# Performance work log

Hardware: AMD Instinct MI355X
Metric: run time of the kernel (lower is better)

## Reference

```python
import jax, jax.numpy as jnp
import numpy as np

EPS = 1e-5
NEG_SLOPE = 0.2

def _conv(x, w, b, stride, pad):
    y = jax.lax.conv_general_dilated(x, w, (stride, stride), ((pad, pad), (pad, pad)),
                                     dimension_numbers=('NCHW', 'OIHW', 'NCHW'))
    return y + b[None, :, None, None]

def _conv_transpose(x, w, b):
    # PyTorch ConvTranspose2d(k=3, s=2, p=1, output_padding=1): equivalent to a
    # lhs-dilated conv with padding (k-1-p, k-1-p+op) = (1, 2). w is stored in the
    # already-flipped OIHW layout (out_ch, in_ch, 3, 3).
    y = jax.lax.conv_general_dilated(x, w, (1, 1), ((1, 2), (1, 2)), lhs_dilation=(2, 2),
                                     dimension_numbers=('NCHW', 'OIHW', 'NCHW'))
    return y + b[None, :, None, None]

def _inorm(x):
    # InstanceNorm2d, affine=False, biased variance over (H, W)
    m = jnp.mean(x, axis=(2, 3), keepdims=True)
    v = jnp.mean((x - m) ** 2, axis=(2, 3), keepdims=True)
    return (x - m) * jax.lax.rsqrt(v + EPS)

def _lrelu(x):
    return jnp.where(x >= 0, x, NEG_SLOPE * x)

def _reflect_pad1(x):
    return jnp.pad(x, ((0, 0), (0, 0), (1, 1), (1, 1)), mode='reflect')


def setup_inputs() -> dict:
    key = jax.random.key(0)
    ks = jax.random.split(key, 12)
    B, H, W, S = 8, 256, 256, 19
    inp = jax.random.normal(ks[0], (B, 3, H, W), dtype=jnp.float32)
    # one-hot semantic map (float, 0/1) like the repo's segmaps
    labels = jax.random.randint(ks[1], (B, H, W), 0, S)
    segmap = jax.nn.one_hot(labels, S, axis=1, dtype=jnp.float32)

    def w(k, o, i):
        return jax.random.normal(k, (o, i, 3, 3), dtype=jnp.float32) * (1.0 / np.sqrt(i * 9))

    return {
        'input': inp, 'segmap': segmap,
        'w0': w(ks[2], 32, 3),    'b0': jnp.zeros((32,), jnp.float32),
        'w1': w(ks[3], 64, 32),   'b1': jnp.zeros((64,), jnp.float32),
        'w2': w(ks[4], 128, 64),  'b2': jnp.zeros((128,), jnp.float32),
        'wt': w(ks[5], 256, 128), 'bt': jnp.zeros((256,), jnp.float32),
        'w3': w(ks[6], 512, 256), 'b3': jnp.zeros((512,), jnp.float32),
    }


def reference(input, segmap, w0, b0, w1, b1, w2, b2, wt, bt, w3, b3):
    # CNN backbone
    x = _conv(_reflect_pad1(input), w0, b0, 1, 0)   # [B,32,256,256]
    x = _lrelu(_inorm(x))
    x = _conv(x, w1, b1, 2, 1)                       # [B,64,128,128]
    x = _lrelu(_inorm(x))
    x = _conv(x, w2, b2, 2, 1)                       # [B,128,64,64]
    x = _lrelu(_inorm(x))
    x = _conv_transpose(x, wt, bt)                   # [B,256,128,128]
    x = _lrelu(_inorm(x))
    codes = jnp.tanh(_conv(_reflect_pad1(x), w3, b3, 1, 0))  # [B,512,128,128]

    # nearest-neighbor downsample of segmap to codes' spatial size (PyTorch floor rule)
    B, C, Hc, Wc = codes.shape
    Hs, Ws = segmap.shape[2], segmap.shape[3]
    hi = (jnp.arange(Hc) * Hs) // Hc
    wi = (jnp.arange(Wc) * Ws) // Wc
    seg = segmap[:, :, hi[:, None], wi[None, :]]     # [B,S,Hc,Wc]

    # fused segment mean pooling (replaces nested masked_select loop)
    m = (seg != 0).astype(codes.dtype)
    sums = jnp.einsum('bchw,bshw->bsc', codes, m)    # [B,S,C]
    cnt = jnp.sum(m, axis=(2, 3))[..., None]          # [B,S,1]
    return jnp.where(cnt > 0, sums / jnp.maximum(cnt, 1.0), 0.0)
```

## Files before the change

### kernel.cpp

```cpp
#include <hip/hip_runtime.h>


#define B 8

typedef __attribute__((ext_vector_type(8))) short short8;
typedef __attribute__((ext_vector_type(4))) float f32x4;

static __device__ __forceinline__ unsigned short f2bf(float f) {
  union { float f; unsigned u; } v;
  v.f = f;
  unsigned r = v.u + 0x7fffu + ((v.u >> 16) & 1u);
  return (unsigned short)(r >> 16);
}
static __device__ __forceinline__ float bf2f(unsigned short h) {
  union { unsigned u; float f; } v;
  v.u = (unsigned)h << 16;
  return v.f;
}
static __device__ __forceinline__ float tanh_fast(float x) {
  float ax = fabsf(x);
  ax = fminf(ax, 20.f);
  const float e = __expf(-2.f * ax);
  const float t = (1.f - e) / (1.f + e);
  return __builtin_copysignf(t, x);
}

static __device__ __forceinline__ void gload_lds16(const unsigned short* g,
                                                   unsigned short* l) {
  __builtin_amdgcn_global_load_lds(
      (const __attribute__((address_space(1))) unsigned int*)(const void*)g,
      (__attribute__((address_space(3))) unsigned int*)(void*)l, 16, 0, 0);
}

__global__ __launch_bounds__(256) void conv0_kernel(
    const float* __restrict__ in, const float* __restrict__ w,
    const float* __restrict__ bias, float* __restrict__ out) {
  __shared__ float sw[32 * 27 + 32];
  for (int i = threadIdx.x; i < 32 * 27; i += 256) sw[i] = w[i];
  if (threadIdx.x < 32) sw[32 * 27 + threadIdx.x] = bias[threadIdx.x];
  __syncthreads();
  const int b = blockIdx.y;
  const int p = blockIdx.x * 256 + threadIdx.x;
  const int y = p >> 8, x = p & 255;
  const float* inb = in + (size_t)b * 3 * 65536;
  float v[27];
#pragma unroll
  for (int c = 0; c < 3; ++c) {
#pragma unroll
    for (int ky = 0; ky < 3; ++ky) {
      int iy = y + ky - 1;
      iy = iy < 0 ? -iy : (iy > 255 ? 510 - iy : iy);
#pragma unroll
      for (int kx = 0; kx < 3; ++kx) {
        int ix = x + kx - 1;
        ix = ix < 0 ? -ix : (ix > 255 ? 510 - ix : ix);
        v[c * 9 + ky * 3 + kx] = inb[c * 65536 + iy * 256 + ix];
      }
    }
  }
  float* ob = out + (size_t)b * 32 * 65536 + p;
#pragma unroll
  for (int co = 0; co < 32; ++co) {
    float a = sw[32 * 27 + co];
#pragma unroll
    for (int k = 0; k < 27; ++k) a = fmaf(v[k], sw[co * 27 + k], a);
    ob[(size_t)co * 65536] = a;
  }
}

__global__ __launch_bounds__(256) void inorm_lrelu_kernel(float* __restrict__ x,
                                                          int HW) {
  const size_t base = (size_t)blockIdx.x * HW;
  float4* p = (float4*)(x + base);
  const int n4 = HW >> 2;
  float s = 0.f, q = 0.f;
  for (int i = threadIdx.x; i < n4; i += 256) {
    float4 v = p[i];
    s += (v.x + v.y) + (v.z + v.w);
    q += (v.x * v.x + v.y * v.y) + (v.z * v.z + v.w * v.w);
  }
  __shared__ float rs[256], rq[256];
  rs[threadIdx.x] = s;
  rq[threadIdx.x] = q;
  __syncthreads();
  for (int st = 128; st > 0; st >>= 1) {
    if (threadIdx.x < st) {
      rs[threadIdx.x] += rs[threadIdx.x + st];
      rq[threadIdx.x] += rq[threadIdx.x + st];
    }
    __syncthreads();
  }
  const float m = rs[0] / (float)HW;
  float var = rq[0] / (float)HW - m * m;
  var = var < 0.f ? 0.f : var;
  const float r = rsqrtf(var + 1e-5f);
  for (int i = threadIdx.x; i < n4; i += 256) {
    float4 v = p[i];
    v.x = (v.x - m) * r; v.x = v.x >= 0.f ? v.x : 0.2f * v.x;
    v.y = (v.y - m) * r; v.y = v.y >= 0.f ? v.y : 0.2f * v.y;
    v.z = (v.z - m) * r; v.z = v.z >= 0.f ? v.z : 0.2f * v.z;
    v.w = (v.w - m) * r; v.w = v.w >= 0.f ? v.w : 0.2f * v.w;
    p[i] = v;
  }
}

__global__ __launch_bounds__(256) void transpose_x0_kernel(
    const float* __restrict__ x0, unsigned short* __restrict__ Xp0) {
  const int b = blockIdx.y;
  const int p0 = blockIdx.x * 64;
  __shared__ unsigned short T[32][66];
  const float* src = x0 + (size_t)b * 32 * 65536;
  const int t = threadIdx.x;
#pragma unroll
  for (int r = 0; r < 8; ++r) {
    const int ci_l = r * 4 + (t >> 6);
    const int p_l = t & 63;
    T[ci_l][p_l] = f2bf(src[(size_t)ci_l * 65536 + p0 + p_l]);
  }
  __syncthreads();
  unsigned short* dst = Xp0 + (size_t)b * 258 * 258 * 32;
  const int p_l = t >> 2;
  const int c0 = (t & 3) * 8;
  union { short8 v; unsigned short u[8]; } pk;
#pragma unroll
  for (int j = 0; j < 8; ++j) pk.u[j] = T[c0 + j][p_l];
  const int p = p0 + p_l;
  const int yy = p >> 8, xx = p & 255;
  *(short8*)(dst + ((size_t)(yy + 1) * 258 + (xx + 1)) * 32 + c0) = pk.v;
}

__global__ __launch_bounds__(256) void zpad0_kernel(unsigned short* __restrict__ Xp0) {
  const int b = blockIdx.x;
  unsigned short* Xb = Xp0 + (size_t)b * 258 * 258 * 32;
  const short8 z = {0, 0, 0, 0, 0, 0, 0, 0};
  for (int i = threadIdx.x; i < 258 * 4; i += 256) {
    const int c = i >> 2, q = (i & 3) * 8;
    *(short8*)(Xb + ((size_t)0 * 258 + c) * 32 + q) = z;
    *(short8*)(Xb + ((size_t)c * 258 + 0) * 32 + q) = z;
  }
}

__global__ __launch_bounds__(256) void w1prep_kernel(const float* __restrict__ w1,
                                                     unsigned short* __restrict__ w1b) {
  const int i = blockIdx.x * 256 + threadIdx.x;
  if (i >= 9 * 64 * 32) return;
  const int e = i & 7, lane = (i >> 3) & 63, cot = (i >> 9) & 3, tap = i >> 11;
  const int co = cot * 16 + (lane & 15);
  const int ci = (lane >> 4) * 8 + e;
  w1b[i] = f2bf(w1[((size_t)co * 32 + ci) * 9 + tap]);
}

__global__ __launch_bounds__(256, 3) void conv1_mfma_kernel(
    const unsigned short* __restrict__ Xp0, const unsigned short* __restrict__ w1b,
    const float* __restrict__ b1, float* __restrict__ x1) {
  const int raw = blockIdx.x;
  const int swz = (raw & 7) * 128 + (raw >> 3);
  const int b = swz >> 7;
  const int oy = swz & 127;

  __shared__ unsigned short Asw1[3084 * 8];

  const int t = threadIdx.x;
  const int lane = t & 63;
  const int wave = t >> 6;
  const int wm = wave >> 1, wn = wave & 1;
  const int lg = lane >> 4, lr = lane & 15;
  const int wslot = wave * 64;

  const unsigned short* Xb = Xp0 + (size_t)b * 258 * 258 * 32;

#pragma unroll
  for (int k = 0; k < 13; ++k) {
    int s;
    bool act = true;
    if (k < 12) s = t + k * 256;
    else { s = 3072 + lane; act = (wave == 0 && lane < 12); }
    const int r = s / 1028, rm = s % 1028, c = rm >> 2, hs = rm & 3;
    const int h = hs ^ ((c >> 1) & 3);
    const unsigned short* gsrc = Xb + ((size_t)(2 * oy + r) * 258 + c) * 32 + h * 8;
    unsigned short* ldst = (k < 12) ? (Asw1 + (size_t)(k * 256 + wslot) * 8)
                                    : (Asw1 + (size_t)3072 * 8);
    if (act) gload_lds16(gsrc, ldst);
  }

  f32x4 acc[4][2];
#pragma unroll
  for (int mt = 0; mt < 4; ++mt)
#pragma unroll
    for (int nt = 0; nt < 2; ++nt) {
      f32x4 z = {0.f, 0.f, 0.f, 0.f};
      acc[mt][nt] = z;
    }
  __syncthreads();

  const unsigned short* w1l = w1b + (size_t)lane * 8;
#pragma unroll
  for (int tap = 0; tap < 9; ++tap) {
    const int ky = tap / 3, kx = tap % 3;
    short8 bf[2];
#pragma unroll
    for (int nt = 0; nt < 2; ++nt)
      bf[nt] = *(const short8*)(w1l + (size_t)(tap * 4 + wn * 2 + nt) * 512);
    short8 af[4];
#pragma unroll
    for (int mt = 0; mt < 4; ++mt) {
      const int c = 2 * (wm * 64 + mt * 16 + lr) + kx;
      const int hh = lg ^ ((c >> 1) & 3);
      af[mt] = *(const short8*)(Asw1 + (size_t)(ky * 1028 + c * 4 + hh) * 8);
    }
#pragma unroll
    for (int nt = 0; nt < 2; ++nt)
#pragma unroll
      for (int mt = 0; mt < 4; ++mt)
        acc[mt][nt] = __builtin_amdgcn_mfma_f32_16x16x32_bf16(
            af[mt], bf[nt], acc[mt][nt], 0, 0, 0);
  }

  float b1v[2];
#pragma unroll
  for (int nt = 0; nt < 2; ++nt) b1v[nt] = b1[wn * 32 + nt * 16 + lr];
#pragma unroll
  for (int mt = 0; mt < 4; ++mt) {
#pragma unroll
    for (int nt = 0; nt < 2; ++nt) {
      const int px = wm * 64 + mt * 16 + lg * 4;
      const int co = wn * 32 + nt * 16 + lr;
      float4 v;
      v.x = acc[mt][nt][0] + b1v[nt];
      v.y = acc[mt][nt][1] + b1v[nt];
      v.z = acc[mt][nt][2] + b1v[nt];
      v.w = acc[mt][nt][3] + b1v[nt];
      *(float4*)(x1 + ((size_t)(b * 64 + co)) * 16384 + oy * 128 + px) = v;
    }
  }
}

__global__ __launch_bounds__(256) void transpose_x1_kernel(
    const float* __restrict__ x1, unsigned short* __restrict__ Xp1) {
  const int b = blockIdx.y;
  const int p0 = blockIdx.x * 64;
  __shared__ unsigned short T[64][66];
  const float* src = x1 + (size_t)b * 64 * 16384;
  const int t = threadIdx.x;
#pragma unroll
  for (int r = 0; r < 16; ++r) {
    const int ci_l = r * 4 + (t >> 6);
    const int p_l = t & 63;
    T[ci_l][p_l] = f2bf(src[(size_t)ci_l * 16384 + p0 + p_l]);
  }
  __syncthreads();
  unsigned short* dst = Xp1 + (size_t)b * 130 * 130 * 64;
#pragma unroll
  for (int r = 0; r < 2; ++r) {
    const int p_l = r * 32 + (t >> 3);
    const int c0 = (t & 7) * 8;
    union { short8 v; unsigned short u[8]; } pk;
#pragma unroll
    for (int j = 0; j < 8; ++j) pk.u[j] = T[c0 + j][p_l];
    const int p = p0 + p_l;
    const int yy = p >> 7, xx = p & 127;
    *(short8*)(dst + ((size_t)(yy + 1) * 130 + (xx + 1)) * 64 + c0) = pk.v;
  }
}

__global__ __launch_bounds__(256) void zpad1_kernel(unsigned short* __restrict__ Xp1) {
  const int b = blockIdx.x;
  unsigned short* Xb = Xp1 + (size_t)b * 130 * 130 * 64;
  const short8 z = {0, 0, 0, 0, 0, 0, 0, 0};
  for (int i = threadIdx.x; i < 130 * 8; i += 256) {
    const int c = i >> 3, q = (i & 7) * 8;
    *(short8*)(Xb + ((size_t)0 * 130 + c) * 64 + q) = z;
    *(short8*)(Xb + ((size_t)c * 130 + 0) * 64 + q) = z;
  }
}

__global__ __launch_bounds__(256) void w2prep_kernel(const float* __restrict__ w2,
                                                     unsigned short* __restrict__ w2b) {
  const int i = blockIdx.x * 256 + threadIdx.x;
  if (i >= 9 * 128 * 64) return;
  const int e = i & 7, lane = (i >> 3) & 63, cc = (i >> 9) & 1;
  const int cot = (i >> 10) & 7, tap = i >> 13;
  const int co = cot * 16 + (lane & 15);
  const int ci = cc * 32 + (lane >> 4) * 8 + e;
  w2b[i] = f2bf(w2[((size_t)co * 64 + ci) * 9 + tap]);
}

__global__ __launch_bounds__(256, 3) void conv2_mfma_kernel(
    const unsigned short* __restrict__ Xp1, const unsigned short* __restrict__ w2b,
    const float* __restrict__ b2, float* __restrict__ x2) {
  const int raw = blockIdx.x;
  const int swz = (raw & 7) * 64 + (raw >> 3);
  const int b = swz >> 6;
  const int oy = swz & 63;

  __shared__ unsigned short Asw2[3096 * 8];

  const int t = threadIdx.x;
  const int lane = t & 63;
  const int wave = t >> 6;
  const int wm = wave >> 1, wn = wave & 1;
  const int lg = lane >> 4, lr = lane & 15;
  const int wslot = wave * 64;

  const unsigned short* Xb = Xp1 + (size_t)b * 130 * 130 * 64;

#pragma unroll
  for (int k = 0; k < 13; ++k) {
    int s;
    bool act = true;
    if (k < 12) s = t + k * 256;
    else { s = 3072 + lane; act = (wave == 0 && lane < 24); }
    const int r = s / 1032, rm = s % 1032, c = rm >> 3, hs = rm & 7;
    const int h = hs ^ ((c >> 1) & 7);
    const unsigned short* gsrc = Xb + ((size_t)(2 * oy + r) * 130 + c) * 64 + h * 8;
    unsigned short* ldst = (k < 12) ? (Asw2 + (size_t)(k * 256 + wslot) * 8)
                                    : (Asw2 + (size_t)3072 * 8);
    if (act) gload_lds16(gsrc, ldst);
  }

  f32x4 acc[2][4];
#pragma unroll
  for (int mt = 0; mt < 2; ++mt)
#pragma unroll
    for (int nt = 0; nt < 4; ++nt) {
      f32x4 z = {0.f, 0.f, 0.f, 0.f};
      acc[mt][nt] = z;
    }
  __syncthreads();

  const unsigned short* w2l = w2b + (size_t)lane * 8;
#pragma unroll
  for (int tap = 0; tap < 9; ++tap) {
    const int ky = tap / 3, kx = tap % 3;
#pragma unroll
    for (int cc = 0; cc < 2; ++cc) {
      short8 bf[4];
#pragma unroll
      for (int nt = 0; nt < 4; ++nt)
        bf[nt] = *(const short8*)(
            w2l + (size_t)((tap * 8 + wn * 4 + nt) * 2 + cc) * 512);
      short8 af[2];
#pragma unroll
      for (int mt = 0; mt < 2; ++mt) {
        const int c = 2 * (wm * 32 + mt * 16 + lr) + kx;
        const int hh = (cc * 4 + lg) ^ ((c >> 1) & 7);
        af[mt] = *(const short8*)(Asw2 + (size_t)(ky * 1032 + c * 8 + hh) * 8);
      }
#pragma unroll
      for (int nt = 0; nt < 4; ++nt)
#pragma unroll
        for (int mt = 0; mt < 2; ++mt)
          acc[mt][nt] = __builtin_amdgcn_mfma_f32_16x16x32_bf16(
              af[mt], bf[nt], acc[mt][nt], 0, 0, 0);
    }
  }

  float b2v[4];
#pragma unroll
  for (int nt = 0; nt < 4; ++nt) b2v[nt] = b2[wn * 64 + nt * 16 + lr];
#pragma unroll
  for (int mt = 0; mt < 2; ++mt) {
#pragma unroll
    for (int nt = 0; nt < 4; ++nt) {
      const int px = wm * 32 + mt * 16 + lg * 4;
      const int co = wn * 64 + nt * 16 + lr;
      float4 v;
      v.x = acc[mt][nt][0] + b2v[nt];
      v.y = acc[mt][nt][1] + b2v[nt];
      v.z = acc[mt][nt][2] + b2v[nt];
      v.w = acc[mt][nt][3] + b2v[nt];
      *(float4*)(x2 + ((size_t)(b * 128 + co)) * 4096 + oy * 64 + px) = v;
    }
  }
}

__global__ __launch_bounds__(256) void transpose_x2_kernel(
    const float* __restrict__ x2, unsigned short* __restrict__ X2p) {
  const int b = blockIdx.y;
  const int p0 = (blockIdx.x & 63) * 64;
  const int ci0 = (blockIdx.x >> 6) * 64;
  __shared__ unsigned short T[64][66];
  const float* src = x2 + (size_t)b * 128 * 4096;
  const int t = threadIdx.x;
#pragma unroll
  for (int r = 0; r < 16; ++r) {
    const int ci_l = r * 4 + (t >> 6);
    const int p_l = t & 63;
    T[ci_l][p_l] = f2bf(src[(size_t)(ci0 + ci_l) * 4096 + p0 + p_l]);
  }
  __syncthreads();
  unsigned short* dst = X2p + (size_t)b * 65 * 65 * 128;
#pragma unroll
  for (int r = 0; r < 2; ++r) {
    const int p_l = r * 32 + (t >> 3);
    const int c0 = (t & 7) * 8;
    union { short8 v; unsigned short u[8]; } pk;
#pragma unroll
    for (int j = 0; j < 8; ++j) pk.u[j] = T[c0 + j][p_l];
    const int p = p0 + p_l;
    const int yy = p >> 6, xx = p & 63;
    *(short8*)(dst + ((size_t)yy * 65 + xx) * 128 + ci0 + c0) = pk.v;
  }
}

__global__ __launch_bounds__(256) void zpad_x2_kernel(unsigned short* __restrict__ X2p) {
  const int b = blockIdx.x;
  unsigned short* Xb = X2p + (size_t)b * 65 * 65 * 128;
  for (int i = threadIdx.x; i < 129 * 128; i += 256) {
    const int j = i >> 7, ci = i & 127;
    size_t off;
    if (j < 65) off = ((size_t)64 * 65 + j) * 128 + ci;
    else off = ((size_t)(j - 65) * 65 + 64) * 128 + ci;
    Xb[off] = 0;
  }
}

__global__ __launch_bounds__(256) void wtprep_kernel(const float* __restrict__ wt,
                                                     unsigned short* __restrict__ Wtb2) {
  const int i = blockIdx.x * 256 + threadIdx.x;
  if (i >= 9 * 256 * 128) return;
  const int e = i & 7, lane = (i >> 3) & 63, c4 = (i >> 9) & 3;
  const int cot = (i >> 11) & 15, tap = i >> 15;
  const int co = cot * 16 + (lane & 15);
  const int ci = c4 * 32 + (lane >> 4) * 8 + e;
  Wtb2[i] = f2bf(wt[((size_t)co * 128 + ci) * 9 + tap]);
}

__global__ __launch_bounds__(256, 3) void convt_mfma_kernel(
    const unsigned short* __restrict__ X2p, const unsigned short* __restrict__ Wtb2,
    const float* __restrict__ bt, unsigned short* __restrict__ Y) {
  const int raw = blockIdx.x;
  const int swz = (raw & 7) * 256 + (raw >> 3);
  const int b = swz >> 8;
  const int rem = swz & 255;
  const int cls = rem >> 6;
  const int sy = rem & 63;
  const int py = cls & 1, px = cls >> 1;

  const int kyA = py ? 0 : 1, kxA = px ? 0 : 1;
  int tk[4], tdy[4], tdx[4];
  int ntaps = 0;
  tk[ntaps] = kyA * 3 + kxA; tdy[ntaps] = 0; tdx[ntaps] = 0; ++ntaps;
  if (px) { tk[ntaps] = kyA * 3 + 2; tdy[ntaps] = 0; tdx[ntaps] = 1; ++ntaps; }
  if (py) { tk[ntaps] = 6 + kxA; tdy[ntaps] = 1; tdx[ntaps] = 0; ++ntaps; }
  if (py && px) { tk[ntaps] = 8; tdy[ntaps] = 1; tdx[ntaps] = 1; ++ntaps; }

  constexpr int CS = 36;
  constexpr int BUFN = 2 * 65 * CS;
  __shared__ unsigned short As2[2 * BUFN];

  const int t = threadIdx.x;
  const int lane = t & 63;
  const int wn = t >> 6;
  const int lg = lane >> 4, lr = lane & 15;
  const int co_w = wn * 64;

  const unsigned short* Xb = X2p + (size_t)b * 65 * 65 * 128;

  int dof0, dof1, dof2;
  const unsigned short *sp0, *sp1, *sp2;
  bool sv2;
  {
    const int i0 = t, i1 = t + 256, i2 = t + 512;
    const int r0 = i0 / 260, c0_ = (i0 % 260) >> 2, h0 = i0 & 3;
    const int r1 = i1 / 260, c1_ = (i1 % 260) >> 2, h1 = i1 & 3;
    sv2 = i2 < 520;
    const int i2c = sv2 ? i2 : 512;
    const int r2 = i2c / 260, c2_ = (i2c % 260) >> 2, h2 = i2c & 3;
    dof0 = (r0 * 65 + c0_) * CS + h0 * 8;
    dof1 = (r1 * 65 + c1_) * CS + h1 * 8;
    dof2 = (r2 * 65 + c2_) * CS + h2 * 8;
    sp0 = Xb + ((size_t)(sy + r0) * 65 + c0_) * 128 + h0 * 8;
    sp1 = Xb + ((size_t)(sy + r1) * 65 + c1_) * 128 + h1 * 8;
    sp2 = Xb + ((size_t)(sy + r2) * 65 + c2_) * 128 + h2 * 8;
  }

  f32x4 acc[4][4];
#pragma unroll
  for (int mt = 0; mt < 4; ++mt)
#pragma unroll
    for (int nt = 0; nt < 4; ++nt) {
      f32x4 z = {0.f, 0.f, 0.f, 0.f};
      acc[mt][nt] = z;
    }

  {
    const short8 a = *(const short8*)sp0;
    const short8 bq = *(const short8*)sp1;
    short8 cq;
    if (sv2) cq = *(const short8*)sp2;
    *(short8*)(As2 + dof0) = a;
    *(short8*)(As2 + dof1) = bq;
    if (sv2) *(short8*)(As2 + dof2) = cq;
  }
  __syncthreads();

  const unsigned short* wlane = Wtb2 + (size_t)lane * 8;

  for (int c8 = 0; c8 < 4; ++c8) {
    short8 n0, n1, n2;
    if (c8 < 3) {
      const int cn = (c8 + 1) * 32;
      n0 = *(const short8*)(sp0 + cn);
      n1 = *(const short8*)(sp1 + cn);
      if (sv2) n2 = *(const short8*)(sp2 + cn);
    }
    const unsigned short* Ab = As2 + (c8 & 1) * BUFN;
    for (int tp = 0; tp < ntaps; ++tp) {
      const int dy = tdy[tp], dx = tdx[tp];
      short8 af[4];
#pragma unroll
      for (int mt = 0; mt < 4; ++mt)
        af[mt] = *(const short8*)(Ab + (dy * 65 + mt * 16 + lr + dx) * CS + lg * 8);
      const unsigned short* wt_ =
          wlane + (size_t)(((tk[tp] * 16 + wn * 4) * 4) + c8) * 512;
#pragma unroll
      for (int nt = 0; nt < 4; ++nt) {
        const short8 bf = *(const short8*)(wt_ + (size_t)nt * (4 * 512));
#pragma unroll
        for (int mt = 0; mt < 4; ++mt)
          acc[mt][nt] = __builtin_amdgcn_mfma_f32_16x16x32_bf16(
              af[mt], bf, acc[mt][nt], 0, 0, 0);
      }
    }
    if (c8 < 3) {
      unsigned short* Db = As2 + ((c8 + 1) & 1) * BUFN;
      *(short8*)(Db + dof0) = n0;
      *(short8*)(Db + dof1) = n1;
      if (sv2) *(short8*)(Db + dof2) = n2;
    }
    __syncthreads();
  }

  const int oy = 2 * sy + py;
  unsigned short* Yb = Y + ((size_t)b * 16384 + (size_t)oy * 128 + px) * 256;
  float bco[4];
#pragma unroll
  for (int nt = 0; nt < 4; ++nt) bco[nt] = bt[co_w + nt * 16 + lr];
#pragma unroll
  for (int mt = 0; mt < 4; ++mt) {
#pragma unroll
    for (int r = 0; r < 4; ++r) {
      const int sx = mt * 16 + lg * 4 + r;
      unsigned short* yp = Yb + (size_t)(2 * sx) * 256 + co_w + lr;
#pragma unroll
      for (int nt = 0; nt < 4; ++nt)
        yp[nt * 16] = f2bf(acc[mt][nt][r] + bco[nt]);
    }
  }
}

__global__ __launch_bounds__(256) void inorm_stats_kernel(
    const unsigned short* __restrict__ Y, float* __restrict__ ssum,
    float* __restrict__ ssq) {
  const int b = blockIdx.y, sl = blockIdx.x;
  const int t = threadIdx.x;
  const int rg = t >> 5;
  const int c0 = (t & 31) * 8;
  const unsigned short* base = Y + ((size_t)b * 16384 + sl * 256) * 256;
  float s[8], q[8];
#pragma unroll
  for (int j = 0; j < 8; ++j) { s[j] = 0.f; q[j] = 0.f; }
  for (int i = 0; i < 32; ++i) {
    union { short8 v; unsigned short u[8]; } pk;
    pk.v = *(const short8*)(base + (size_t)(rg + i * 8) * 256 + c0);
#pragma unroll
    for (int j = 0; j < 8; ++j) {
      const float v = bf2f(pk.u[j]);
      s[j] += v;
      q[j] += v * v;
    }
  }
  __shared__ float sm[2][8][256];
#pragma unroll
  for (int j = 0; j < 8; ++j) {
    sm[0][rg][c0 + j] = s[j];
    sm[1][rg][c0 + j] = q[j];
  }
  __syncthreads();
  float ts = 0.f, tq = 0.f;
#pragma unroll
  for (int g = 0; g < 8; ++g) {
    ts += sm[0][g][t];
    tq += sm[1][g][t];
  }
  atomicAdd(&ssum[b * 256 + t], ts);
  atomicAdd(&ssq[b * 256 + t], tq);
}

__global__ __launch_bounds__(256) void inorm_apply_kernel(
    const unsigned short* __restrict__ Y, const float* __restrict__ ssum,
    const float* __restrict__ ssq, unsigned short* __restrict__ Xpad) {
  const int b = blockIdx.y, sl = blockIdx.x;
  const int t = threadIdx.x;
  const int rg = t >> 5;
  const int c0 = (t & 31) * 8;
  float m[8], r[8];
#pragma unroll
  for (int j = 0; j < 8; ++j) {
    const float mm = ssum[b * 256 + c0 + j] * (1.f / 16384.f);
    float var = ssq[b * 256 + c0 + j] * (1.f / 16384.f) - mm * mm;
    var = var < 0.f ? 0.f : var;
    m[j] = mm;
    r[j] = rsqrtf(var + 1e-5f);
  }
  const unsigned short* base = Y + ((size_t)b * 16384 + sl * 256) * 256;
  unsigned short* dstb = Xpad + (size_t)b * 130 * 130 * 256;
  for (int i = 0; i < 32; ++i) {
    const int row = sl * 256 + rg + i * 8;
    const int yy = row >> 7, xx = row & 127;
    union { short8 v; unsigned short u[8]; } pk;
    pk.v = *(const short8*)(base + (size_t)(rg + i * 8) * 256 + c0);
#pragma unroll
    for (int j = 0; j < 8; ++j) {
      float v = bf2f(pk.u[j]);
      v = (v - m[j]) * r[j];
      v = v >= 0.f ? v : 0.2f * v;
      pk.u[j] = f2bf(v);
    }
    *(short8*)(dstb + ((size_t)(yy + 1) * 130 + (xx + 1)) * 256 + c0) = pk.v;
  }
}

__global__ __launch_bounds__(256) void pad_rows_kernel(unsigned short* __restrict__ Xp) {
  const int b = blockIdx.x >> 1, side = blockIdx.x & 1;
  unsigned short* Xb = Xp + (size_t)b * 130 * 130 * 256;
  const int dr = side ? 129 : 0, sr = side ? 127 : 2;
  for (int i = threadIdx.x; i < 4096; i += 256) {
    const int c = 1 + (i >> 5), o = (i & 31) * 8;
    *(short8*)(Xb + ((size_t)dr * 130 + c) * 256 + o) =
        *(const short8*)(Xb + ((size_t)sr * 130 + c) * 256 + o);
  }
}
__global__ __launch_bounds__(256) void pad_cols_kernel(unsigned short* __restrict__ Xp) {
  const int b = blockIdx.x >> 1, side = blockIdx.x & 1;
  unsigned short* Xb = Xp + (size_t)b * 130 * 130 * 256;
  const int dc = side ? 129 : 0, sc = side ? 127 : 2;
  for (int i = threadIdx.x; i < 130 * 32; i += 256) {
    const int r = i >> 5, o = (i & 31) * 8;
    *(short8*)(Xb + ((size_t)r * 130 + dc) * 256 + o) =
        *(const short8*)(Xb + ((size_t)r * 130 + sc) * 256 + o);
  }
}

__global__ __launch_bounds__(256) void wprep_kernel(const float* __restrict__ w3,
                                                    unsigned short* __restrict__ Wb2) {
  const int i = blockIdx.x * 256 + threadIdx.x;
  if (i >= 9 * 512 * 256) return;
  const int e = i & 7, lane = (i >> 3) & 63, c8 = (i >> 9) & 7;
  const int cot = (i >> 12) & 31, tap = i >> 17;
  const int co = cot * 16 + (lane & 15);
  const int ci = c8 * 32 + (lane >> 4) * 8 + e;
  Wb2[i] = f2bf(w3[((size_t)co * 256 + ci) * 9 + tap]);
}

__global__ __launch_bounds__(256) void label_kernel(
    const float* __restrict__ segmap, int* __restrict__ labels,
    float* __restrict__ cnt) {
  const int b = blockIdx.y;
  const int p = blockIdx.x * 256 + threadIdx.x;
  const int i = p >> 7, j = p & 127;
  const float* sp = segmap + (size_t)b * 19 * 65536 + (2 * i) * 256 + 2 * j;
  int lab = 0;
#pragma unroll
  for (int s = 0; s < 19; ++s)
    if (sp[(size_t)s * 65536] != 0.f) lab = s;
  labels[b * 16384 + p] = lab;
  atomicAdd(&cnt[b * 19 + lab], 1.0f);
}

__global__ __launch_bounds__(256, 3) void conv3_mfma_pool_kernel(
    const unsigned short* __restrict__ Xpad, const unsigned short* __restrict__ Wb2,
    const float* __restrict__ bias, const int* __restrict__ labels,
    float* __restrict__ sums) {
  const int raw = blockIdx.x;
  const int swz = (raw & 7) * 512 + (raw >> 3);
  const int b = swz >> 9;
  const int rem = swz & 511;
  const int y = rem >> 2;
  const int coq = rem & 3;

  constexpr int SLOTS = 1600;
  __shared__ unsigned short Asw[2 * SLOTS * 8];
  float* lsum = (float*)Asw;

  const int t = threadIdx.x;
  const int lane = t & 63;
  const int wave = t >> 6;
  const int wm = wave >> 1;
  const int wn = wave & 1;
  const int lg = lane >> 4, lr = lane & 15;
  const int co_w = coq * 128 + wn * 64;

  const unsigned short* Xb = Xpad + (size_t)b * 130 * 130 * 256;

  const unsigned short* sp[7];
  {
#pragma unroll
    for (int k = 0; k < 7; ++k) {
      int s;
      if (k < 6) s = t + k * 256;
      else s = (t < 24) ? (1536 + t) : 1536;
      const int r = s / 520, rm = s % 520, c = rm >> 2, hs = rm & 3;
      const int E = r * 130 + c;
      const int h = hs ^ ((E >> 1) & 3);
      sp[k] = Xb + ((size_t)(y + r) * 130 + c) * 256 + h * 8;
    }
  }

  f32x4 acc[4][4];
#pragma unroll
  for (int mt = 0; mt < 4; ++mt)
#pragma unroll
    for (int nt = 0; nt < 4; ++nt) {
      f32x4 z = {0.f, 0.f, 0.f, 0.f};
      acc[mt][nt] = z;
    }

  const unsigned short* wlane = Wb2 + (size_t)lane * 8;

  const int wslot = wave * 64;
#define STAGE(bufSel, off)                                                   \
  {                                                                          \
    unsigned short* base_ = Asw + (bufSel) * (SLOTS * 8);                    \
    gload_lds16(sp[0] + (off), base_ + (size_t)wslot * 8);                   \
    gload_lds16(sp[1] + (off), base_ + (size_t)(wslot + 256) * 8);           \
    gload_lds16(sp[2] + (off), base_ + (size_t)(wslot + 512) * 8);           \
    gload_lds16(sp[3] + (off), base_ + (size_t)(wslot + 768) * 8);           \
    gload_lds16(sp[4] + (off), base_ + (size_t)(wslot + 1024) * 8);          \
    gload_lds16(sp[5] + (off), base_ + (size_t)(wslot + 1280) * 8);          \
    if (wave == 0 && lane < 24)                                              \
      gload_lds16(sp[6] + (off), base_ + (size_t)1536 * 8);                  \
  }

  STAGE(0, 0)
  __syncthreads();

  for (int c8 = 0; c8 < 8; ++c8) {
    if (c8 < 7) STAGE((c8 + 1) & 1, (c8 + 1) * 32)
    const unsigned short* Ab = Asw + (c8 & 1) * (SLOTS * 8);
#pragma unroll
    for (int ky = 0; ky < 3; ++ky) {
#pragma unroll
      for (int kx = 0; kx < 3; ++kx) {
        const unsigned short* wt_ =
            wlane +
            (size_t)(((ky * 3 + kx) * 32 + coq * 8 + wn * 4) * 8 + c8) * 512;
        short8 bfv[4];
#pragma unroll
        for (int nt = 0; nt < 4; ++nt)
          bfv[nt] = *(const short8*)(wt_ + (size_t)nt * (8 * 512));
        short8 af[4];
#pragma unroll
        for (int mt = 0; mt < 4; ++mt) {
          const int E = ky * 130 + wm * 64 + mt * 16 + lr + kx;
          const int hh = lg ^ ((E >> 1) & 3);
          af[mt] = *(const short8*)(Ab + (size_t)E * 32 + hh * 8);
        }
#pragma unroll
        for (int nt = 0; nt < 4; ++nt) {
#pragma unroll
          for (int mt = 0; mt < 4; ++mt)
            acc[mt][nt] = __builtin_amdgcn_mfma_f32_16x16x32_bf16(
                af[mt], bfv[nt], acc[mt][nt], 0, 0, 0);
        }
      }
    }
    __syncthreads();
  }
#undef STAGE

  for (int i = t; i < 19 * 128; i += 256) lsum[i] = 0.f;
  __syncthreads();

  const int* labp = labels + b * 16384 + y * 128;
  float bco[4];
#pragma unroll
  for (int nt = 0; nt < 4; ++nt) bco[nt] = bias[co_w + nt * 16 + lr];
#pragma unroll
  for (int mt = 0; mt < 4; ++mt) {
#pragma unroll
    for (int r = 0; r < 4; ++r) {
      const int lab = labp[wm * 64 + mt * 16 + lg * 4 + r];
#pragma unroll
      for (int nt = 0; nt < 4; ++nt) {
        const float v = tanh_fast(acc[mt][nt][r] + bco[nt]);
        atomicAdd(&lsum[lab * 128 + wn * 64 + nt * 16 + lr], v);
      }
    }
  }
  __syncthreads();
  for (int i = t; i < 19 * 128; i += 256) {
    const float v = lsum[i];
    if (v != 0.f) {
      const int sI = i >> 7, c = i & 127;
      atomicAdd(&sums[((size_t)b * 19 + sI) * 512 + coq * 128 + c], v);
    }
  }
}

__global__ __launch_bounds__(256) void finalize_kernel(
    const float* __restrict__ sums, const float* __restrict__ cnt,
    float* __restrict__ out) {
  const int i = blockIdx.x * 256 + threadIdx.x;
  if (i >= B * 19 * 512) return;
  const int bs = i >> 9;
  const float c = cnt[bs];
  out[i] = c > 0.f ? sums[i] / fmaxf(c, 1.f) : 0.f;
}

extern "C" void kernel_launch(void* const* d_in, const int* in_sizes, int n_in,
                              void* d_out, int out_size, void* d_ws,
                              size_t ws_size, hipStream_t stream) {
  const float* input = (const float*)d_in[0];
  const float* segmap = (const float*)d_in[1];
  const float* w0 = (const float*)d_in[2];
  const float* b0 = (const float*)d_in[3];
  const float* w1 = (const float*)d_in[4];
  const float* b1 = (const float*)d_in[5];
  const float* w2 = (const float*)d_in[6];
  const float* b2 = (const float*)d_in[7];
  const float* wt = (const float*)d_in[8];
  const float* bt = (const float*)d_in[9];
  const float* w3 = (const float*)d_in[10];
  const float* b3 = (const float*)d_in[11];
  float* out = (float*)d_out;

  float* ws = (float*)d_ws;
  float* x0 = ws;
  float* x1 = x0 + 16777216;
  float* x2 = x1 + 8388608;
  unsigned short* X2p = (unsigned short*)(x2 + 4194304);
  unsigned short* Y = X2p + 4326400;
  float* sums = (float*)(Y + 33554432);
  float* cnt = sums + 77824;
  float* ssum = cnt + 152;
  float* ssq = ssum + 2048;
  int* labels = (int*)(ssq + 2048);
  unsigned short* Wb2 = (unsigned short*)(labels + 131072);
  unsigned short* Wtb2 = Wb2 + 1179648;
  unsigned short* w1b = Wtb2 + 294912;
  unsigned short* w2b = w1b + 18432;
  unsigned short* Xpad = (unsigned short*)ws;
  unsigned short* Xp0 = Y;
  unsigned short* Xp1 = Y + 17040384;

  hipMemsetAsync(sums, 0, (77824 + 152 + 2048 + 2048) * sizeof(float), stream);

  wprep_kernel<<<dim3((9 * 512 * 256 + 255) / 256), 256, 0, stream>>>(w3, Wb2);
  wtprep_kernel<<<dim3((9 * 256 * 128 + 255) / 256), 256, 0, stream>>>(wt, Wtb2);
  w1prep_kernel<<<dim3((9 * 64 * 32 + 255) / 256), 256, 0, stream>>>(w1, w1b);
  w2prep_kernel<<<dim3((9 * 128 * 64 + 255) / 256), 256, 0, stream>>>(w2, w2b);

  conv0_kernel<<<dim3(256, B), 256, 0, stream>>>(input, w0, b0, x0);
  inorm_lrelu_kernel<<<dim3(B * 32), 256, 0, stream>>>(x0, 65536);
  transpose_x0_kernel<<<dim3(1024, B), 256, 0, stream>>>(x0, Xp0);
  zpad0_kernel<<<dim3(B), 256, 0, stream>>>(Xp0);
  conv1_mfma_kernel<<<dim3(1024), 256, 0, stream>>>(Xp0, w1b, b1, x1);
  inorm_lrelu_kernel<<<dim3(B * 64), 256, 0, stream>>>(x1, 16384);
  transpose_x1_kernel<<<dim3(256, B), 256, 0, stream>>>(x1, Xp1);
  zpad1_kernel<<<dim3(B), 256, 0, stream>>>(Xp1);
  conv2_mfma_kernel<<<dim3(512), 256, 0, stream>>>(Xp1, w2b, b2, x2);
  inorm_lrelu_kernel<<<dim3(B * 128), 256, 0, stream>>>(x2, 4096);
  transpose_x2_kernel<<<dim3(128, B), 256, 0, stream>>>(x2, X2p);
  zpad_x2_kernel<<<dim3(B), 256, 0, stream>>>(X2p);
  convt_mfma_kernel<<<dim3(2048), 256, 0, stream>>>(X2p, Wtb2, bt, Y);
  inorm_stats_kernel<<<dim3(64, B), 256, 0, stream>>>(Y, ssum, ssq);
  inorm_apply_kernel<<<dim3(64, B), 256, 0, stream>>>(Y, ssum, ssq, Xpad);
  pad_rows_kernel<<<dim3(2 * B), 256, 0, stream>>>(Xpad);
  pad_cols_kernel<<<dim3(2 * B), 256, 0, stream>>>(Xpad);
  label_kernel<<<dim3(64, B), 256, 0, stream>>>(segmap, labels, cnt);
  conv3_mfma_pool_kernel<<<dim3(4096), 256, 0, stream>>>(Xpad, Wb2, b3, labels, sums);
  finalize_kernel<<<dim3((B * 19 * 512 + 255) / 256), 256, 0, stream>>>(sums, cnt, out);
}
```

Measured before the change: 961.8 us.

## Write bf16 NHWC directly from convs, fuse instance-norm stats into epilogues

conv0, conv1 and conv2 now write bf16 channels-last padded tensors directly. This removes the fp32 NCHW intermediates and the separate transpose kernels. Instance norm for these layers is split into a pixel-major stats kernel with atomics plus an in-place apply kernel. The transposed conv accumulates per-channel sum and sum-of-squares in its epilogue, which drops the separate stats pass, and its input staging now uses direct global-to-LDS loads into a swizzled layout without double buffering. The risks are that stats are now computed from bf16-rounded values, and conv1/conv2 issue scattered 2-byte stores.

```diff
diff --git a/kernel.cpp b/kernel.cpp
--- a/kernel.cpp
+++ b/kernel.cpp
@@ -34,7 +34,7 @@
 
 __global__ __launch_bounds__(256) void conv0_kernel(
     const float* __restrict__ in, const float* __restrict__ w,
-    const float* __restrict__ bias, float* __restrict__ out) {
+    const float* __restrict__ bias, unsigned short* __restrict__ Xp0) {
   __shared__ float sw[32 * 27 + 32];
   for (int i = threadIdx.x; i < 32 * 27; i += 256) sw[i] = w[i];
   if (threadIdx.x < 32) sw[32 * 27 + threadIdx.x] = bias[threadIdx.x];
@@ -58,75 +58,100 @@
       }
     }
   }
-  float* ob = out + (size_t)b * 32 * 65536 + p;
-#pragma unroll
-  for (int co = 0; co < 32; ++co) {
-    float a = sw[32 * 27 + co];
-#pragma unroll
-    for (int k = 0; k < 27; ++k) a = fmaf(v[k], sw[co * 27 + k], a);
-    ob[(size_t)co * 65536] = a;
-  }
-}
-
-__global__ __launch_bounds__(256) void inorm_lrelu_kernel(float* __restrict__ x,
-                                                          int HW) {
-  const size_t base = (size_t)blockIdx.x * HW;
-  float4* p = (float4*)(x + base);
-  const int n4 = HW >> 2;
-  float s = 0.f, q = 0.f;
-  for (int i = threadIdx.x; i < n4; i += 256) {
-    float4 v = p[i];
-    s += (v.x + v.y) + (v.z + v.w);
-    q += (v.x * v.x + v.y * v.y) + (v.z * v.z + v.w * v.w);
-  }
-  __shared__ float rs[256], rq[256];
-  rs[threadIdx.x] = s;
-  rq[threadIdx.x] = q;
+  unsigned short* ob =
+      Xp0 + ((size_t)b * 258 * 258 + (size_t)(y + 1) * 258 + (x + 1)) * 32;
+#pragma unroll
+  for (int q = 0; q < 4; ++q) {
+    union { short8 v8; unsigned short u[8]; } pk;
+#pragma unroll
+    for (int j = 0; j < 8; ++j) {
+      const int co = q * 8 + j;
+      float a = sw[32 * 27 + co];
+#pragma unroll
+      for (int k = 0; k < 27; ++k) a = fmaf(v[k], sw[co * 27 + k], a);
+      pk.u[j] = f2bf(a);
+    }
+    *(short8*)(ob + q * 8) = pk.v8;
+  }
+}
+
+template <int C, int WLOG, int STR, int SH, int ITER>
+__global__ __launch_bounds__(256) void stats_px_kernel(
+    const unsigned short* __restrict__ X, float* __restrict__ ssum,
+    float* __restrict__ ssq) {
+  constexpr int G = C / 8;
+  constexpr int R = 256 / G;
+  const int b = blockIdx.y;
+  const int t = threadIdx.x;
+  const int rg = t / G;
+  const int cg = (t % G) * 8;
+  const int px0 = blockIdx.x * (R * ITER);
+  const unsigned short* Xb = X + (size_t)b * STR * STR * C;
+  float s[8], q[8];
+#pragma unroll
+  for (int j = 0; j < 8; ++j) { s[j] = 0.f; q[j] = 0.f; }
+  for (int i = 0; i < ITER; ++i) {
+    const int p = px0 + i * R + rg;
+    const int yy = p >> WLOG, xx = p & ((1 << WLOG) - 1);
+    union { short8 v8; unsigned short u[8]; } pk;
+    pk.v8 = *(const short8*)(Xb + ((size_t)(yy + SH) * STR + (xx + SH)) * C + cg);
+#pragma unroll
+    for (int j = 0; j < 8; ++j) {
+      const float v = bf2f(pk.u[j]);
+      s[j] += v;
+      q[j] += v * v;
+    }
+  }
+  __shared__ float sm[2][R][C];
+#pragma unroll
+  for (int j = 0; j < 8; ++j) {
+    sm[0][rg][cg + j] = s[j];
+    sm[1][rg][cg + j] = q[j];
+  }
   __syncthreads();
-  for (int st = 128; st > 0; st >>= 1) {
-    if (threadIdx.x < st) {
-      rs[threadIdx.x] += rs[threadIdx.x + st];
-      rq[threadIdx.x] += rq[threadIdx.x + st];
-    }
-    __syncthreads();
-  }
-  const float m = rs[0] / (float)HW;
-  float var = rq[0] / (float)HW - m * m;
-  var = var < 0.f ? 0.f : var;
-  const float r = rsqrtf(var + 1e-5f);
-  for (int i = threadIdx.x; i < n4; i += 256) {
-    float4 v = p[i];
-    v.x = (v.x - m) * r; v.x = v.x >= 0.f ? v.x : 0.2f * v.x;
-    v.y = (v.y - m) * r; v.y = v.y >= 0.f ? v.y : 0.2f * v.y;
-    v.z = (v.z - m) * r; v.z = v.z >= 0.f ? v.z : 0.2f * v.z;
-    v.w = (v.w - m) * r; v.w = v.w >= 0.f ? v.w : 0.2f * v.w;
-    p[i] = v;
-  }
-}
-
-__global__ __launch_bounds__(256) void transpose_x0_kernel(
-    const float* __restrict__ x0, unsigned short* __restrict__ Xp0) {
+  if (t < C) {
+    float ts = 0.f, tq = 0.f;
+    for (int g2 = 0; g2 < R; ++g2) {
+      ts += sm[0][g2][t];
+      tq += sm[1][g2][t];
+    }
+    atomicAdd(&ssum[b * C + t], ts);
+    atomicAdd(&ssq[b * C + t], tq);
+  }
+}
+
+template <int C, int WLOG, int STR, int SH>
+__global__ __launch_bounds__(256) void apply_px_kernel(
+    unsigned short* __restrict__ X, const float* __restrict__ ssum,
+    const float* __restrict__ ssq) {
+  constexpr int G = C / 8;
   const int b = blockIdx.y;
-  const int p0 = blockIdx.x * 64;
-  __shared__ unsigned short T[32][66];
-  const float* src = x0 + (size_t)b * 32 * 65536;
-  const int t = threadIdx.x;
-#pragma unroll
-  for (int r = 0; r < 8; ++r) {
-    const int ci_l = r * 4 + (t >> 6);
-    const int p_l = t & 63;
-    T[ci_l][p_l] = f2bf(src[(size_t)ci_l * 65536 + p0 + p_l]);
-  }
-  __syncthreads();
-  unsigned short* dst = Xp0 + (size_t)b * 258 * 258 * 32;
-  const int p_l = t >> 2;
-  const int c0 = (t & 3) * 8;
-  union { short8 v; unsigned short u[8]; } pk;
-#pragma unroll
-  for (int j = 0; j < 8; ++j) pk.u[j] = T[c0 + j][p_l];
-  const int p = p0 + p_l;
-  const int yy = p >> 8, xx = p & 255;
-  *(short8*)(dst + ((size_t)(yy + 1) * 258 + (xx + 1)) * 32 + c0) = pk.v;
+  const int i = blockIdx.x * 256 + threadIdx.x;
+  const int p = i / G;
+  const int cg = (i % G) * 8;
+  const int yy = p >> WLOG, xx = p & ((1 << WLOG) - 1);
+  constexpr float inv = 1.f / (float)(1 << (2 * WLOG));
+  float m[8], r[8];
+#pragma unroll
+  for (int j = 0; j < 8; ++j) {
+    const float mm = ssum[b * C + cg + j] * inv;
+    float var = ssq[b * C + cg + j] * inv - mm * mm;
+    var = var < 0.f ? 0.f : var;
+    m[j] = mm;
+    r[j] = rsqrtf(var + 1e-5f);
+  }
+  unsigned short* pp =
+      X + (size_t)b * STR * STR * C + ((size_t)(yy + SH) * STR + (xx + SH)) * C + cg;
+  union { short8 v8; unsigned short u[8]; } pk;
+  pk.v8 = *(const short8*)pp;
+#pragma unroll
+  for (int j = 0; j < 8; ++j) {
+    float v = bf2f(pk.u[j]);
+    v = (v - m[j]) * r[j];
+    v = v >= 0.f ? v : 0.2f * v;
+    pk.u[j] = f2bf(v);
+  }
+  *(short8*)pp = pk.v8;
 }
 
 __global__ __launch_bounds__(256) void zpad0_kernel(unsigned short* __restrict__ Xp0) {
@@ -152,7 +177,7 @@
 
 __global__ __launch_bounds__(256, 3) void conv1_mfma_kernel(
     const unsigned short* __restrict__ Xp0, const unsigned short* __restrict__ w1b,
-    const float* __restrict__ b1, float* __restrict__ x1) {
+    const float* __restrict__ b1, unsigned short* __restrict__ Xp1) {
   const int raw = blockIdx.x;
   const int swz = (raw & 7) * 128 + (raw >> 3);
   const int b = swz >> 7;
@@ -219,47 +244,19 @@
   float b1v[2];
 #pragma unroll
   for (int nt = 0; nt < 2; ++nt) b1v[nt] = b1[wn * 32 + nt * 16 + lr];
+  unsigned short* yb =
+      Xp1 + ((size_t)b * 130 * 130 + (size_t)(oy + 1) * 130) * 64;
 #pragma unroll
   for (int mt = 0; mt < 4; ++mt) {
 #pragma unroll
-    for (int nt = 0; nt < 2; ++nt) {
-      const int px = wm * 64 + mt * 16 + lg * 4;
-      const int co = wn * 32 + nt * 16 + lr;
-      float4 v;
-      v.x = acc[mt][nt][0] + b1v[nt];
-      v.y = acc[mt][nt][1] + b1v[nt];
-      v.z = acc[mt][nt][2] + b1v[nt];
-      v.w = acc[mt][nt][3] + b1v[nt];
-      *(float4*)(x1 + ((size_t)(b * 64 + co)) * 16384 + oy * 128 + px) = v;
-    }
-  }
-}
-
-__global__ __launch_bounds__(256) void transpose_x1_kernel(
-    const float* __restrict__ x1, unsigned short* __restrict__ Xp1) {
-  const int b = blockIdx.y;
-  const int p0 = blockIdx.x * 64;
-  __shared__ unsigned short T[64][66];
-  const float* src = x1 + (size_t)b * 64 * 16384;
-  const int t = threadIdx.x;
-#pragma unroll
-  for (int r = 0; r < 16; ++r) {
-    const int ci_l = r * 4 + (t >> 6);
-    const int p_l = t & 63;
-    T[ci_l][p_l] = f2bf(src[(size_t)ci_l * 16384 + p0 + p_l]);
-  }
-  __syncthreads();
-  unsigned short* dst = Xp1 + (size_t)b * 130 * 130 * 64;
-#pragma unroll
-  for (int r = 0; r < 2; ++r) {
-    const int p_l = r * 32 + (t >> 3);
-    const int c0 = (t & 7) * 8;
-    union { short8 v; unsigned short u[8]; } pk;
-#pragma unroll
-    for (int j = 0; j < 8; ++j) pk.u[j] = T[c0 + j][p_l];
-    const int p = p0 + p_l;
-    const int yy = p >> 7, xx = p & 127;
-    *(short8*)(dst + ((size_t)(yy + 1) * 130 + (xx + 1)) * 64 + c0) = pk.v;
+    for (int r = 0; r < 4; ++r) {
+      const int px_ = wm * 64 + mt * 16 + lg * 4 + r;
+#pragma unroll
+      for (int nt = 0; nt < 2; ++nt) {
+        const int co = wn * 32 + nt * 16 + lr;
+        yb[(size_t)(px_ + 1) * 64 + co] = f2bf(acc[mt][nt][r] + b1v[nt]);
+      }
+    }
   }
 }
 
@@ -287,7 +284,7 @@
 
 __global__ __launch_bounds__(256, 3) void conv2_mfma_kernel(
     const unsigned short* __restrict__ Xp1, const unsigned short* __restrict__ w2b,
-    const float* __restrict__ b2, float* __restrict__ x2) {
+    const float* __restrict__ b2, unsigned short* __restrict__ X2p) {
   const int raw = blockIdx.x;
   const int swz = (raw & 7) * 64 + (raw >> 3);
   const int b = swz >> 6;
@@ -358,48 +355,18 @@
   float b2v[4];
 #pragma unroll
   for (int nt = 0; nt < 4; ++nt) b2v[nt] = b2[wn * 64 + nt * 16 + lr];
+  unsigned short* yb = X2p + ((size_t)b * 65 * 65 + (size_t)oy * 65) * 128;
 #pragma unroll
   for (int mt = 0; mt < 2; ++mt) {
 #pragma unroll
-    for (int nt = 0; nt < 4; ++nt) {
-      const int px = wm * 32 + mt * 16 + lg * 4;
-      const int co = wn * 64 + nt * 16 + lr;
-      float4 v;
-      v.x = acc[mt][nt][0] + b2v[nt];
-      v.y = acc[mt][nt][1] + b2v[nt];
-      v.z = acc[mt][nt][2] + b2v[nt];
-      v.w = acc[mt][nt][3] + b2v[nt];
-      *(float4*)(x2 + ((size_t)(b * 128 + co)) * 4096 + oy * 64 + px) = v;
-    }
-  }
-}
-
-__global__ __launch_bounds__(256) void transpose_x2_kernel(
-    const float* __restrict__ x2, unsigned short* __restrict__ X2p) {
-  const int b = blockIdx.y;
-  const int p0 = (blockIdx.x & 63) * 64;
-  const int ci0 = (blockIdx.x >> 6) * 64;
-  __shared__ unsigned short T[64][66];
-  const float* src = x2 + (size_t)b * 128 * 4096;
-  const int t = threadIdx.x;
-#pragma unroll
-  for (int r = 0; r < 16; ++r) {
-    const int ci_l = r * 4 + (t >> 6);
-    const int p_l = t & 63;
-    T[ci_l][p_l] = f2bf(src[(size_t)(ci0 + ci_l) * 4096 + p0 + p_l]);
-  }
-  __syncthreads();
-  unsigned short* dst = X2p + (size_t)b * 65 * 65 * 128;
-#pragma unroll
-  for (int r = 0; r < 2; ++r) {
-    const int p_l = r * 32 + (t >> 3);
-    const int c0 = (t & 7) * 8;
-    union { short8 v; unsigned short u[8]; } pk;
-#pragma unroll
-    for (int j = 0; j < 8; ++j) pk.u[j] = T[c0 + j][p_l];
-    const int p = p0 + p_l;
-    const int yy = p >> 6, xx = p & 63;
-    *(short8*)(dst + ((size_t)yy * 65 + xx) * 128 + ci0 + c0) = pk.v;
+    for (int r = 0; r < 4; ++r) {
+      const int px_ = wm * 32 + mt * 16 + lg * 4 + r;
+#pragma unroll
+      for (int nt = 0; nt < 4; ++nt) {
+        const int co = wn * 64 + nt * 16 + lr;
+        yb[(size_t)px_ * 128 + co] = f2bf(acc[mt][nt][r] + b2v[nt]);
+      }
+    }
   }
 }
 
@@ -428,7 +395,8 @@
 
 __global__ __launch_bounds__(256, 3) void convt_mfma_kernel(
     const unsigned short* __restrict__ X2p, const unsigned short* __restrict__ Wtb2,
-    const float* __restrict__ bt, unsigned short* __restrict__ Y) {
+    const float* __restrict__ bt, unsigned short* __restrict__ Y,
+    float* __restrict__ ssumY, float* __restrict__ ssqY) {
   const int raw = blockIdx.x;
   const int swz = (raw & 7) * 256 + (raw >> 3);
   const int b = swz >> 8;
@@ -445,9 +413,7 @@
   if (py) { tk[ntaps] = 6 + kxA; tdy[ntaps] = 1; tdx[ntaps] = 0; ++ntaps; }
   if (py && px) { tk[ntaps] = 8; tdy[ntaps] = 1; tdx[ntaps] = 1; ++ntaps; }
 
-  constexpr int CS = 36;
-  constexpr int BUFN = 2 * 65 * CS;
-  __shared__ unsigned short As2[2 * BUFN];
+  __shared__ unsigned short As2[2080 * 8];
 
   const int t = threadIdx.x;
   const int lane = t & 63;
@@ -457,22 +423,20 @@
 
   const unsigned short* Xb = X2p + (size_t)b * 65 * 65 * 128;
 
-  int dof0, dof1, dof2;
-  const unsigned short *sp0, *sp1, *sp2;
-  bool sv2;
-  {
-    const int i0 = t, i1 = t + 256, i2 = t + 512;
-    const int r0 = i0 / 260, c0_ = (i0 % 260) >> 2, h0 = i0 & 3;
-    const int r1 = i1 / 260, c1_ = (i1 % 260) >> 2, h1 = i1 & 3;
-    sv2 = i2 < 520;
-    const int i2c = sv2 ? i2 : 512;
-    const int r2 = i2c / 260, c2_ = (i2c % 260) >> 2, h2 = i2c & 3;
-    dof0 = (r0 * 65 + c0_) * CS + h0 * 8;
-    dof1 = (r1 * 65 + c1_) * CS + h1 * 8;
-    dof2 = (r2 * 65 + c2_) * CS + h2 * 8;
-    sp0 = Xb + ((size_t)(sy + r0) * 65 + c0_) * 128 + h0 * 8;
-    sp1 = Xb + ((size_t)(sy + r1) * 65 + c1_) * 128 + h1 * 8;
-    sp2 = Xb + ((size_t)(sy + r2) * 65 + c2_) * 128 + h2 * 8;
+#pragma unroll
+  for (int k = 0; k < 9; ++k) {
+    int s;
+    bool act = true;
+    if (k < 8) s = k * 256 + t;
+    else { s = 2048 + lane; act = (wn == 0 && lane < 32); }
+    const int r = s >= 1040 ? 1 : 0;
+    const int rm = s - r * 1040;
+    const int c = rm >> 4, hs = rm & 15;
+    const int g = hs ^ (c & 7);
+    const unsigned short* gsrc = Xb + ((size_t)(sy + r) * 65 + c) * 128 + g * 8;
+    unsigned short* ldst =
+        As2 + (size_t)(k < 8 ? (k * 256 + wn * 64) : 2048) * 8;
+    if (act) gload_lds16(gsrc, ldst);
   }
 
   f32x4 acc[4][4];
@@ -483,35 +447,19 @@
       f32x4 z = {0.f, 0.f, 0.f, 0.f};
       acc[mt][nt] = z;
     }
-
-  {
-    const short8 a = *(const short8*)sp0;
-    const short8 bq = *(const short8*)sp1;
-    short8 cq;
-    if (sv2) cq = *(const short8*)sp2;
-    *(short8*)(As2 + dof0) = a;
-    *(short8*)(As2 + dof1) = bq;
-    if (sv2) *(short8*)(As2 + dof2) = cq;
-  }
   __syncthreads();
 
   const unsigned short* wlane = Wtb2 + (size_t)lane * 8;
-
   for (int c8 = 0; c8 < 4; ++c8) {
-    short8 n0, n1, n2;
-    if (c8 < 3) {
-      const int cn = (c8 + 1) * 32;
-      n0 = *(const short8*)(sp0 + cn);
-      n1 = *(const short8*)(sp1 + cn);
-      if (sv2) n2 = *(const short8*)(sp2 + cn);
-    }
-    const unsigned short* Ab = As2 + (c8 & 1) * BUFN;
     for (int tp = 0; tp < ntaps; ++tp) {
       const int dy = tdy[tp], dx = tdx[tp];
       short8 af[4];
 #pragma unroll
-      for (int mt = 0; mt < 4; ++mt)
-        af[mt] = *(const short8*)(Ab + (dy * 65 + mt * 16 + lr + dx) * CS + lg * 8);
+      for (int mt = 0; mt < 4; ++mt) {
+        const int c = mt * 16 + lr + dx;
+        const int hs = (c8 * 4 + lg) ^ (c & 7);
+        af[mt] = *(const short8*)(As2 + (size_t)((dy * 65 + c) * 16 + hs) * 8);
+      }
       const unsigned short* wt_ =
           wlane + (size_t)(((tk[tp] * 16 + wn * 4) * 4) + c8) * 512;
 #pragma unroll
@@ -523,20 +471,17 @@
               af[mt], bf, acc[mt][nt], 0, 0, 0);
       }
     }
-    if (c8 < 3) {
-      unsigned short* Db = As2 + ((c8 + 1) & 1) * BUFN;
-      *(short8*)(Db + dof0) = n0;
-      *(short8*)(Db + dof1) = n1;
-      if (sv2) *(short8*)(Db + dof2) = n2;
-    }
-    __syncthreads();
   }
 
   const int oy = 2 * sy + py;
   unsigned short* Yb = Y + ((size_t)b * 16384 + (size_t)oy * 128 + px) * 256;
-  float bco[4];
-#pragma unroll
-  for (int nt = 0; nt < 4; ++nt) bco[nt] = bt[co_w + nt * 16 + lr];
+  float bco[4], sS[4], sQ[4];
+#pragma unroll
+  for (int nt = 0; nt < 4; ++nt) {
+    bco[nt] = bt[co_w + nt * 16 + lr];
+    sS[nt] = 0.f;
+    sQ[nt] = 0.f;
+  }
 #pragma unroll
   for (int mt = 0; mt < 4; ++mt) {
 #pragma unroll
@@ -544,48 +489,28 @@
       const int sx = mt * 16 + lg * 4 + r;
       unsigned short* yp = Yb + (size_t)(2 * sx) * 256 + co_w + lr;
 #pragma unroll
-      for (int nt = 0; nt < 4; ++nt)
-        yp[nt * 16] = f2bf(acc[mt][nt][r] + bco[nt]);
-    }
-  }
-}
-
-__global__ __launch_bounds__(256) void inorm_stats_kernel(
-    const unsigned short* __restrict__ Y, float* __restrict__ ssum,
-    float* __restrict__ ssq) {
-  const int b = blockIdx.y, sl = blockIdx.x;
-  const int t = threadIdx.x;
-  const int rg = t >> 5;
-  const int c0 = (t & 31) * 8;
-  const unsigned short* base = Y + ((size_t)b * 16384 + sl * 256) * 256;
-  float s[8], q[8];
-#pragma unroll
-  for (int j = 0; j < 8; ++j) { s[j] = 0.f; q[j] = 0.f; }
-  for (int i = 0; i < 32; ++i) {
-    union { short8 v; unsigned short u[8]; } pk;
-    pk.v = *(const short8*)(base + (size_t)(rg + i * 8) * 256 + c0);
-#pragma unroll
-    for (int j = 0; j < 8; ++j) {
-      const float v = bf2f(pk.u[j]);
-      s[j] += v;
-      q[j] += v * v;
-    }
-  }
-  __shared__ float sm[2][8][256];
-#pragma unroll
-  for (int j = 0; j < 8; ++j) {
-    sm[0][rg][c0 + j] = s[j];
-    sm[1][rg][c0 + j] = q[j];
-  }
-  __syncthreads();
-  float ts = 0.f, tq = 0.f;
-#pragma unroll
-  for (int g = 0; g < 8; ++g) {
-    ts += sm[0][g][t];
-    tq += sm[1][g][t];
-  }
-  atomicAdd(&ssum[b * 256 + t], ts);
-  atomicAdd(&ssq[b * 256 + t], tq);
+      for (int nt = 0; nt < 4; ++nt) {
+        const float v = acc[mt][nt][r] + bco[nt];
+        yp[nt * 16] = f2bf(v);
+        sS[nt] += v;
+        sQ[nt] += v * v;
+      }
+    }
+  }
+#pragma unroll
+  for (int nt = 0; nt < 4; ++nt) {
+    sS[nt] += __shfl_xor(sS[nt], 16);
+    sS[nt] += __shfl_xor(sS[nt], 32);
+    sQ[nt] += __shfl_xor(sQ[nt], 16);
+    sQ[nt] += __shfl_xor(sQ[nt], 32);
+  }
+  if (lg == 0) {
+#pragma unroll
+    for (int nt = 0; nt < 4; ++nt) {
+      atomicAdd(&ssumY[b * 256 + co_w + nt * 16 + lr], sS[nt]);
+      atomicAdd(&ssqY[b * 256 + co_w + nt * 16 + lr], sQ[nt]);
+    }
+  }
 }
 
 __global__ __launch_bounds__(256) void inorm_apply_kernel(
@@ -826,47 +751,51 @@
   const float* b3 = (const float*)d_in[11];
   float* out = (float*)d_out;
 
-  float* ws = (float*)d_ws;
-  float* x0 = ws;
-  float* x1 = x0 + 16777216;
-  float* x2 = x1 + 8388608;
-  unsigned short* X2p = (unsigned short*)(x2 + 4194304);
+  unsigned short* Xpad = (unsigned short*)d_ws;
+  unsigned short* X2p = Xpad + 34611200;
   unsigned short* Y = X2p + 4326400;
   float* sums = (float*)(Y + 33554432);
   float* cnt = sums + 77824;
-  float* ssum = cnt + 152;
-  float* ssq = ssum + 2048;
-  int* labels = (int*)(ssq + 2048);
+  float* ssum0 = cnt + 152;
+  float* ssq0 = ssum0 + 256;
+  float* ssum1 = ssq0 + 256;
+  float* ssq1 = ssum1 + 512;
+  float* ssum2 = ssq1 + 512;
+  float* ssq2 = ssum2 + 1024;
+  float* ssumY = ssq2 + 1024;
+  float* ssqY = ssumY + 2048;
+  int* labels = (int*)(ssqY + 2048);
   unsigned short* Wb2 = (unsigned short*)(labels + 131072);
   unsigned short* Wtb2 = Wb2 + 1179648;
   unsigned short* w1b = Wtb2 + 294912;
   unsigned short* w2b = w1b + 18432;
-  unsigned short* Xpad = (unsigned short*)ws;
   unsigned short* Xp0 = Y;
   unsigned short* Xp1 = Y + 17040384;
 
-  hipMemsetAsync(sums, 0, (77824 + 152 + 2048 + 2048) * sizeof(float), stream);
+  hipMemsetAsync(sums, 0, (77824 + 152 + 7680) * sizeof(float), stream);
 
   wprep_kernel<<<dim3((9 * 512 * 256 + 255) / 256), 256, 0, stream>>>(w3, Wb2);
   wtprep_kernel<<<dim3((9 * 256 * 128 + 255) / 256), 256, 0, stream>>>(wt, Wtb2);
   w1prep_kernel<<<dim3((9 * 64 * 32 + 255) / 256), 256, 0, stream>>>(w1, w1b);
   w2prep_kernel<<<dim3((9 * 128 * 64 + 255) / 256), 256, 0, stream>>>(w2, w2b);
 
-  conv0_kernel<<<dim3(256, B), 256, 0, stream>>>(input, w0, b0, x0);
-  inorm_lrelu_kernel<<<dim3(B * 32), 256, 0, stream>>>(x0, 65536);
-  transpose_x0_kernel<<<dim3(1024, B), 256, 0, stream>>>(x0, Xp0);
+  conv0_kernel<<<dim3(256, B), 256, 0, stream>>>(input, w0, b0, Xp0);
   zpad0_kernel<<<dim3(B), 256, 0, stream>>>(Xp0);
-  conv1_mfma_kernel<<<dim3(1024), 256, 0, stream>>>(Xp0, w1b, b1, x1);
-  inorm_lrelu_kernel<<<dim3(B * 64), 256, 0, stream>>>(x1, 16384);
-  transpose_x1_kernel<<<dim3(256, B), 256, 0, stream>>>(x1, Xp1);
+  stats_px_kernel<32, 8, 258, 1, 16><<<dim3(64, B), 256, 0, stream>>>(Xp0, ssum0, ssq0);
+  apply_px_kernel<32, 8, 258, 1><<<dim3(1024, B), 256, 0, stream>>>(Xp0, ssum0, ssq0);
+
+  conv1_mfma_kernel<<<dim3(1024), 256, 0, stream>>>(Xp0, w1b, b1, Xp1);
   zpad1_kernel<<<dim3(B), 256, 0, stream>>>(Xp1);
-  conv2_mfma_kernel<<<dim3(512), 256, 0, stream>>>(Xp1, w2b, b2, x2);
-  inorm_lrelu_kernel<<<dim3(B * 128), 256, 0, stream>>>(x2, 4096);
-  transpose_x2_kernel<<<dim3(128, B), 256, 0, stream>>>(x2, X2p);
+  stats_px_kernel<64, 7, 130, 1, 16><<<dim3(32, B), 256, 0, stream>>>(Xp1, ssum1, ssq1);
+  apply_px_kernel<64, 7, 130, 1><<<dim3(512, B), 256, 0, stream>>>(Xp1, ssum1, ssq1);
+
+  conv2_mfma_kernel<<<dim3(512), 256, 0, stream>>>(Xp1, w2b, b2, X2p);
   zpad_x2_kernel<<<dim3(B), 256, 0, stream>>>(X2p);
-  convt_mfma_kernel<<<dim3(2048), 256, 0, stream>>>(X2p, Wtb2, bt, Y);
-  inorm_stats_kernel<<<dim3(64, B), 256, 0, stream>>>(Y, ssum, ssq);
-  inorm_apply_kernel<<<dim3(64, B), 256, 0, stream>>>(Y, ssum, ssq, Xpad);
+  stats_px_kernel<128, 6, 65, 0, 16><<<dim3(16, B), 256, 0, stream>>>(X2p, ssum2, ssq2);
+  apply_px_kernel<128, 6, 65, 0><<<dim3(256, B), 256, 0, stream>>>(X2p, ssum2, ssq2);
+
+  convt_mfma_kernel<<<dim3(2048), 256, 0, stream>>>(X2p, Wtb2, bt, Y, ssumY, ssqY);
+  inorm_apply_kernel<<<dim3(64, B), 256, 0, stream>>>(Y, ssumY, ssqY, Xpad);
   pad_rows_kernel<<<dim3(2 * B), 256, 0, stream>>>(Xpad);
   pad_cols_kernel<<<dim3(2 * B), 256, 0, stream>>>(Xpad);
   label_kernel<<<dim3(64, B), 256, 0, stream>>>(segmap, labels, cnt);
```

Measured after the change: 912.7 us, median of 2. 1.05x faster.
